# Optimization experiments

Measured on AMD Instinct MI355X. Metric: run time of the kernel, lower is better.

## Reference

```python
import jax, jax.numpy as jnp
import numpy as np

D_MODEL = 1024
NUM_HEADS = 16
D_K = D_MODEL // NUM_HEADS


def setup_inputs() -> dict:
    key = jax.random.key(0)
    ks = jax.random.split(key, 12)
    B, S = 2, 2048
    s = 1.0 / np.sqrt(D_MODEL)
    inp = {
        "query": jax.random.normal(ks[0], (B, S, D_MODEL), jnp.float32),
        "key": jax.random.normal(ks[1], (B, S, D_MODEL), jnp.float32),
        "value": jax.random.normal(ks[2], (B, S, D_MODEL), jnp.float32),
        "w_q": jax.random.normal(ks[3], (D_MODEL, D_MODEL), jnp.float32) * s,
        "b_q": jax.random.normal(ks[4], (D_MODEL,), jnp.float32) * 0.01,
        "w_k": jax.random.normal(ks[5], (D_MODEL, D_MODEL), jnp.float32) * s,
        "b_k": jax.random.normal(ks[6], (D_MODEL,), jnp.float32) * 0.01,
        "w_v": jax.random.normal(ks[7], (D_MODEL, D_MODEL), jnp.float32) * s,
        "b_v": jax.random.normal(ks[8], (D_MODEL,), jnp.float32) * 0.01,
        "w_o": jax.random.normal(ks[9], (D_MODEL, D_MODEL), jnp.float32) * s,
        "b_o": jax.random.normal(ks[10], (D_MODEL,), jnp.float32) * 0.01,
    }
    return inp


def _split_heads(x):
    # [B, S, d_model] -> [B, H, S, d_k]
    B, S, _ = x.shape
    return x.reshape(B, S, NUM_HEADS, D_K).transpose(0, 2, 1, 3)


def reference(query, key, value, w_q, b_q, w_k, b_k, w_v, b_v, w_o, b_o):
    B, S, _ = query.shape
    Q = _split_heads(query @ w_q.T + b_q)
    K = _split_heads(key @ w_k.T + b_k)
    V = _split_heads(value @ w_v.T + b_v)
    scale = 1.0 / jnp.sqrt(jnp.asarray(D_K, Q.dtype))
    scores = jnp.einsum("bhqd,bhkd->bhqk", Q, K) * scale  # [B,H,S,S]
    attn = jax.nn.softmax(scores, axis=-1)
    ctx = jnp.einsum("bhqk,bhkd->bhqd", attn, V)
    ctx = ctx.transpose(0, 2, 1, 3).reshape(B, S, D_MODEL)
    return ctx @ w_o.T + b_o
```

## Files before the change

### kernel.cpp

```cpp
#include <hip/hip_runtime.h>
#include <hip/hip_bf16.h>
#include <stdint.h>

#define D_MODEL 1024
#define NHEAD   16
#define DK      64
#define SEQ     2048
#define BATCH   2

using bf16 = __bf16;
typedef __bf16 bf16x8 __attribute__((ext_vector_type(8)));
typedef float  f32x4  __attribute__((ext_vector_type(4)));
typedef float  f32x16 __attribute__((ext_vector_type(16)));
typedef unsigned uintx2 __attribute__((ext_vector_type(2)));

__device__ __forceinline__ unsigned short f2bf(float x) {
  return __builtin_bit_cast(unsigned short, (__bf16)x);
}
__device__ __forceinline__ unsigned pk2bf(float a, float b) {
  return (unsigned)f2bf(a) | ((unsigned)f2bf(b) << 16);
}
__device__ __forceinline__ float uasf(unsigned x) {
  return __builtin_bit_cast(float, x);
}
__device__ __forceinline__ unsigned fasu(float x) {
  return __builtin_bit_cast(unsigned, x);
}

__device__ __forceinline__ void gld_lds16(const void* g, void* l) {
  __builtin_amdgcn_global_load_lds(
      (const __attribute__((address_space(1))) void*)g,
      (__attribute__((address_space(3))) void*)l, 16, 0, 0);
}

__device__ __forceinline__ float xhalf_sum(float x) {
  uintx2 r = __builtin_amdgcn_permlane32_swap(fasu(x), fasu(x), false, false);
  return uasf(r[0]) + uasf(r[1]);
}

#define MHA_PACK(sv, off, dst)                                           \
  {                                                                      \
    float e0 = __builtin_amdgcn_exp2f(sv[off + 0]);                      \
    float e1 = __builtin_amdgcn_exp2f(sv[off + 1]);                      \
    float e2 = __builtin_amdgcn_exp2f(sv[off + 2]);                      \
    float e3 = __builtin_amdgcn_exp2f(sv[off + 3]);                      \
    float e4 = __builtin_amdgcn_exp2f(sv[off + 4]);                      \
    float e5 = __builtin_amdgcn_exp2f(sv[off + 5]);                      \
    float e6 = __builtin_amdgcn_exp2f(sv[off + 6]);                      \
    float e7 = __builtin_amdgcn_exp2f(sv[off + 7]);                      \
    ps += ((e0 + e1) + (e2 + e3)) + ((e4 + e5) + (e6 + e7));             \
    unsigned c0 = pk2bf(e0, e1), c1 = pk2bf(e2, e3);                     \
    unsigned c2 = pk2bf(e4, e5), c3 = pk2bf(e6, e7);                     \
    uintx2 r02 = __builtin_amdgcn_permlane32_swap(c0, c2, false, false); \
    uintx2 r13 = __builtin_amdgcn_permlane32_swap(c1, c3, false, false); \
    uint4 w; w.x = r02[0]; w.y = r13[0]; w.z = r02[1]; w.w = r13[1];     \
    dst = __builtin_bit_cast(bf16x8, w);                                 \
  }

struct ConvArgs {
  const float* src[7];
  bf16* dst[7];
};

__global__ __launch_bounds__(256) void convert_f32_bf16(ConvArgs a) {
  int v = blockIdx.x * 256 + threadIdx.x;
  int seg, off;
  if (v < 3 * 1048576) { seg = v >> 20; off = v & (1048576 - 1); }
  else { int u = v - 3 * 1048576; seg = 3 + (u >> 18); off = u & (262144 - 1); }
  float4 f = ((const float4*)a.src[seg])[off];
  ushort4 o;
  o.x = f2bf(f.x); o.y = f2bf(f.y); o.z = f2bf(f.z); o.w = f2bf(f.w);
  ((ushort4*)a.dst[seg])[off] = o;
}

__device__ __forceinline__ void gemm_qkv_core(
    const bf16* __restrict__ A, const bf16* __restrict__ B,
    const float* __restrict__ bias, bf16* __restrict__ Cout,
    int mode, int bx, int by, float oscale, char* lds) {
  constexpr int BUF = 16384;
  constexpr int NKT = D_MODEL / 32;
  const int tid  = threadIdx.x;
  const int lane = tid & 63;
  const int wave = tid >> 6;
  const int wr = wave >> 1, wc = wave & 1;
  const int t = lane >> 4, q = lane & 15;

  f32x4 acc[4][4];
#pragma unroll
  for (int i = 0; i < 4; ++i)
#pragma unroll
    for (int j = 0; j < 4; ++j) acc[i][j] = (f32x4){0.f, 0.f, 0.f, 0.f};

  const char* Abase = (const char*)(A + (size_t)bx * 128 * D_MODEL);
  const char* Bbase = (const char*)(B + (size_t)by * 128 * D_MODEL);

  const char* gA[2]; char* sA[2]; const char* gB[2]; char* sB[2];
#pragma unroll
  for (int i = 0; i < 2; ++i) {
    int c = tid + i * 256, row = c >> 2;
    int src = ((c & 3) * 16) ^ ((row & 3) << 4);
    gA[i] = Abase + (size_t)row * (D_MODEL * 2) + src;
    sA[i] = lds + c * 16;
    gB[i] = Bbase + (size_t)row * (D_MODEL * 2) + src;
    sB[i] = lds + 8192 + c * 16;
  }

  const char* aA[4]; const char* aB[4];
#pragma unroll
  for (int f = 0; f < 4; ++f) {
    int ra = wr * 64 + f * 16 + q;
    aA[f] = lds + ra * 64 + ((t * 16) ^ ((q & 3) << 4));
    int rb = wc * 64 + f * 16 + q;
    aB[f] = lds + 8192 + rb * 64 + ((t * 16) ^ ((q & 3) << 4));
  }

#pragma unroll
  for (int i = 0; i < 2; ++i) { gld_lds16(gA[i], sA[i]); gld_lds16(gB[i], sB[i]); }
#pragma unroll
  for (int i = 0; i < 2; ++i) {
    gld_lds16(gA[i] + 64, sA[i] + BUF); gld_lds16(gB[i] + 64, sB[i] + BUF);
  }
  asm volatile("s_waitcnt vmcnt(4)" ::: "memory");
  __builtin_amdgcn_s_barrier();

#pragma unroll
  for (int kt = 0; kt < NKT; ++kt) {
    const int CUR = (kt % 3) * BUF;
    if (kt + 2 < NKT) {
      const int NB = ((kt + 2) % 3) * BUF;
#pragma unroll
      for (int i = 0; i < 2; ++i) {
        gld_lds16(gA[i] + (kt + 2) * 64, sA[i] + NB);
        gld_lds16(gB[i] + (kt + 2) * 64, sB[i] + NB);
      }
    }
    bf16x8 af[4], bfv[4];
#pragma unroll
    for (int f = 0; f < 4; ++f) af[f]  = *(const bf16x8*)(aA[f] + CUR);
#pragma unroll
    for (int f = 0; f < 4; ++f) bfv[f] = *(const bf16x8*)(aB[f] + CUR);
    __builtin_amdgcn_s_setprio(1);
#pragma unroll
    for (int fm = 0; fm < 4; ++fm)
#pragma unroll
      for (int fn = 0; fn < 4; ++fn)
        acc[fm][fn] = __builtin_amdgcn_mfma_f32_16x16x32_bf16(
            af[fm], bfv[fn], acc[fm][fn], 0, 0, 0);
    __builtin_amdgcn_s_setprio(0);
    if (kt + 2 < NKT)      asm volatile("s_waitcnt vmcnt(4)" ::: "memory");
    else if (kt + 1 < NKT) asm volatile("s_waitcnt vmcnt(0)" ::: "memory");
    __builtin_amdgcn_s_barrier();
  }

#pragma unroll
  for (int fm = 0; fm < 4; ++fm)
#pragma unroll
    for (int fn = 0; fn < 4; ++fn)
#pragma unroll
      for (int jj = 0; jj < 4; ++jj) {
        int m = bx * 128 + wr * 64 + fm * 16 + t * 4 + jj;
        int n = by * 128 + wc * 64 + fn * 16 + q;
        float v = acc[fm][fn][jj];
        if (mode == 0) {
          v = (v + bias[n]) * oscale;
          int b = m >> 11, s = m & (SEQ - 1), h = n >> 6, d = n & 63;
          Cout[(((size_t)(b * NHEAD + h)) * SEQ + s) * DK + d] = (bf16)v;
        } else {
          v += bias[m];
          int h = m >> 6, d = m & 63, b = n >> 11, s = n & (SEQ - 1);
          Cout[(((size_t)(b * NHEAD + h)) * DK + d) * SEQ + s] = (bf16)v;
        }
      }
}

struct QkvArgs {
  const bf16* A[3]; const bf16* B[3]; const float* bias[3]; bf16* out[3];
};

__global__ __launch_bounds__(256, 2) void gemm_qkv(QkvArgs a) {
  __shared__ char lds[3 * 16384];
  int z = blockIdx.z;
  int mode = (z == 2) ? 1 : 0;
  int bx = (z == 2) ? blockIdx.y : blockIdx.x;
  int by = (z == 2) ? blockIdx.x : blockIdx.y;
  float osc = (z == 0) ? 0.18033688011112042f : 1.0f;
  gemm_qkv_core(a.A[z], a.B[z], a.bias[z], a.out[z], mode, bx, by, osc, lds);
}

template <int BM>
__device__ __forceinline__ void gemm_core(
    const bf16* __restrict__ A, const bf16* __restrict__ B,
    const float* __restrict__ bias, float* __restrict__ Cout,
    int bx, int by, char* lds) {
  constexpr int FM   = BM / 32;
  constexpr int ACH  = BM / 32;
  constexpr int HALF = BM * 128 + 16384;
  const int tid  = threadIdx.x;
  const int lane = tid & 63;
  const int wave = tid >> 6;
  const int wr = wave >> 1, wc = wave & 1;
  const int t = lane >> 4, q = lane & 15;

  f32x4 acc[FM][4];
#pragma unroll
  for (int i = 0; i < FM; ++i)
#pragma unroll
    for (int j = 0; j < 4; ++j) acc[i][j] = (f32x4){0.f, 0.f, 0.f, 0.f};

  const char* Abase = (const char*)(A + (size_t)bx * BM * D_MODEL);
  const char* Bbase = (const char*)(B + (size_t)by * 128 * D_MODEL);

  const char* gA[ACH]; char* sA[ACH];
  const char* gB[4];   char* sB[4];
#pragma unroll
  for (int i = 0; i < ACH; ++i) {
    int c = tid + i * 256, row = c >> 3;
    int src = ((c & 7) * 16) ^ ((row & 7) << 4);
    gA[i] = Abase + (size_t)row * (D_MODEL * 2) + src;
    sA[i] = lds + c * 16;
  }
#pragma unroll
  for (int i = 0; i < 4; ++i) {
    int c = tid + i * 256, row = c >> 3;
    int src = ((c & 7) * 16) ^ ((row & 7) << 4);
    gB[i] = Bbase + (size_t)row * (D_MODEL * 2) + src;
    sB[i] = lds + BM * 128 + c * 16;
  }

  const char* aA[FM][2]; const char* aB[4][2];
#pragma unroll
  for (int f = 0; f < FM; ++f)
#pragma unroll
    for (int ks = 0; ks < 2; ++ks) {
      int ra = wr * (BM / 2) + f * 16 + q;
      aA[f][ks] = lds + ra * 128 + ((ks * 64 + t * 16) ^ ((q & 7) << 4));
    }
#pragma unroll
  for (int f = 0; f < 4; ++f)
#pragma unroll
    for (int ks = 0; ks < 2; ++ks) {
      int rb = wc * 64 + f * 16 + q;
      aB[f][ks] = lds + BM * 128 + rb * 128 + ((ks * 64 + t * 16) ^ ((q & 7) << 4));
    }

#pragma unroll
  for (int i = 0; i < ACH; ++i) gld_lds16(gA[i], sA[i]);
#pragma unroll
  for (int i = 0; i < 4; ++i)  gld_lds16(gB[i], sB[i]);
  __syncthreads();

  auto ktile = [&](int kt, int CUR) {
    if (kt + 1 < D_MODEL / 64) {
      int NXT = CUR ^ HALF;
#pragma unroll
      for (int i = 0; i < ACH; ++i) gld_lds16(gA[i] + (kt + 1) * 128, sA[i] + NXT);
#pragma unroll
      for (int i = 0; i < 4; ++i)  gld_lds16(gB[i] + (kt + 1) * 128, sB[i] + NXT);
    }
#pragma unroll
    for (int ks = 0; ks < 2; ++ks) {
      bf16x8 af[FM], bfv[4];
#pragma unroll
      for (int f = 0; f < FM; ++f) af[f] = *(const bf16x8*)(aA[f][ks] + CUR);
#pragma unroll
      for (int f = 0; f < 4; ++f)  bfv[f] = *(const bf16x8*)(aB[f][ks] + CUR);
      __builtin_amdgcn_s_setprio(1);
#pragma unroll
      for (int fm = 0; fm < FM; ++fm)
#pragma unroll
        for (int fn = 0; fn < 4; ++fn)
          acc[fm][fn] = __builtin_amdgcn_mfma_f32_16x16x32_bf16(
              af[fm], bfv[fn], acc[fm][fn], 0, 0, 0);
      __builtin_amdgcn_s_setprio(0);
    }
    __syncthreads();
  };
  for (int kt = 0; kt < D_MODEL / 64; kt += 2) {
    ktile(kt, 0);
    ktile(kt + 1, HALF);
  }

#pragma unroll
  for (int fm = 0; fm < FM; ++fm)
#pragma unroll
    for (int fn = 0; fn < 4; ++fn)
#pragma unroll
      for (int jj = 0; jj < 4; ++jj) {
        int m = bx * BM + wr * (BM / 2) + fm * 16 + t * 4 + jj;
        int n = by * 128 + wc * 64 + fn * 16 + q;
        Cout[(size_t)m * D_MODEL + n] = acc[fm][fn][jj] + bias[n];
      }
}

__global__ __launch_bounds__(256, 2) void gemm_o(
    const bf16* __restrict__ A, const bf16* __restrict__ B,
    const float* __restrict__ bias, float* __restrict__ Cout) {
  __shared__ char lds[2 * (64 * 128 + 16384)];
  gemm_core<64>(A, B, bias, Cout, blockIdx.x, blockIdx.y, lds);
}

__global__ __launch_bounds__(512, 2) void flash_attn(
    const bf16* __restrict__ Qh, const bf16* __restrict__ Kh,
    const bf16* __restrict__ Vt, bf16* __restrict__ ctx) {
  __shared__ char lds[65536];
  const int tid  = threadIdx.x;
  const int lane = tid & 63;
  const int wave = tid >> 6;
  const int lo = lane & 31;
  const int hi = lane >> 5;
  const int grp = wave >> 2;
  const int wq  = wave & 3;
  const int bh = blockIdx.x;
  const int q0 = blockIdx.y * 128 + wq * 32;

  const bf16* Qb = Qh + (size_t)bh * SEQ * DK;
  const char* Kb = (const char*)(Kh + (size_t)bh * SEQ * DK) + grp * 1024 * 128;
  const char* Vb = (const char*)(Vt + (size_t)bh * DK * SEQ) + grp * 1024 * 2;
  char* Kg = lds + grp * 16384;
  char* Vg = lds + 32768 + grp * 16384;

  bf16x8 qf[4];
#pragma unroll
  for (int c = 0; c < 4; ++c)
    qf[c] = *(const bf16x8*)(Qb + (size_t)(q0 + lo) * DK + c * 16 + hi * 8);

  const int tg = tid & 255;
  const int srow = tg >> 3;
  const int ssrc = ((tg & 7) * 16) ^ ((srow & 7) << 4);
  const char* gK0 = Kb + (size_t)srow * 128 + ssrc;
  const char* gK1 = Kb + (size_t)(srow + 32) * 128 + ssrc;
  const char* gV0 = Vb + (size_t)srow * 4096 + ssrc;
  const char* gV1 = Vb + (size_t)(srow + 32) * 4096 + ssrc;
  char* sK0 = Kg + tg * 16;
  char* sK1 = Kg + 4096 + tg * 16;
  char* sV0 = Vg + tg * 16;
  char* sV1 = Vg + 4096 + tg * 16;

  const int key = (lo & 7) << 4;
  const char* KA[4]; const char* VA[4];
#pragma unroll
  for (int c = 0; c < 4; ++c) {
    int o = (((2 * c + hi) * 16) ^ key) + lo * 128;
    KA[c] = Kg + o;
    VA[c] = Vg + o;
  }

  f32x16 acc0 = {}, acc1 = {};
  float lsum = 0.f;

  gld_lds16(gK0, sK0); gld_lds16(gK1, sK1);
  gld_lds16(gV0, sV0); gld_lds16(gV1, sV1);
  __syncthreads();

  auto tile = [&](int kt, int CUR) {
    if (kt + 1 < 16) {
      int nb = CUR ^ 8192;
      gld_lds16(gK0 + (kt + 1) * 8192, sK0 + nb);
      gld_lds16(gK1 + (kt + 1) * 8192, sK1 + nb);
      gld_lds16(gV0 + (kt + 1) * 128,  sV0 + nb);
      gld_lds16(gV1 + (kt + 1) * 128,  sV1 + nb);
    }

    float ps = 0.f;
    bf16x8 pa[4];

    {
      bf16x8 kf[4];
#pragma unroll
      for (int c = 0; c < 4; ++c) kf[c] = *(const bf16x8*)(KA[c] + CUR);
      f32x16 s0 = {};
      __builtin_amdgcn_s_setprio(1);
#pragma unroll
      for (int c = 0; c < 4; ++c)
        s0 = __builtin_amdgcn_mfma_f32_32x32x16_bf16(kf[c], qf[c], s0, 0, 0, 0);
      __builtin_amdgcn_s_setprio(0);
      MHA_PACK(s0, 0, pa[0]);
      MHA_PACK(s0, 8, pa[1]);
    }

    {
      bf16x8 kf[4];
#pragma unroll
      for (int c = 0; c < 4; ++c) kf[c] = *(const bf16x8*)(KA[c] + CUR + 4096);
      f32x16 s1 = {};
      __builtin_amdgcn_s_setprio(1);
#pragma unroll
      for (int c = 0; c < 4; ++c)
        s1 = __builtin_amdgcn_mfma_f32_32x32x16_bf16(kf[c], qf[c], s1, 0, 0, 0);
      __builtin_amdgcn_s_setprio(0);
      MHA_PACK(s1, 0, pa[2]);
      MHA_PACK(s1, 8, pa[3]);
    }
    lsum += ps;

    bf16x8 vf[2][4];
#pragma unroll
    for (int ks = 0; ks < 4; ++ks) {
      vf[0][ks] = *(const bf16x8*)(VA[ks] + CUR);
      vf[1][ks] = *(const bf16x8*)(VA[ks] + CUR + 4096);
    }
    __builtin_amdgcn_s_setprio(1);
#pragma unroll
    for (int ks = 0; ks < 4; ++ks) {
      acc0 = __builtin_amdgcn_mfma_f32_32x32x16_bf16(pa[ks], vf[0][ks], acc0, 0, 0, 0);
      acc1 = __builtin_amdgcn_mfma_f32_32x32x16_bf16(pa[ks], vf[1][ks], acc1, 0, 0, 0);
    }
    __builtin_amdgcn_s_setprio(0);

    __syncthreads();
  };

  for (int kt = 0; kt < 16; kt += 2) {
    tile(kt, 0);
    tile(kt + 1, 8192);
  }

  float lrun = xhalf_sum(lsum);

  float* lsh = (float*)lds;
  float* U1  = (float*)(lds + 4096);
  if (hi == 0) lsh[grp * 128 + wq * 32 + lo] = lrun;
  if (grp == 1) {
    float* dst = U1 + (size_t)(wq * 64 + lane) * 33;
#pragma unroll
    for (int r = 0; r < 16; ++r) { dst[r] = acc0[r]; dst[16 + r] = acc1[r]; }
  }
  __syncthreads();
  if (grp == 0) {
    const float* src = U1 + (size_t)(wq * 64 + lane) * 33;
    int b = bh >> 4, h = bh & 15;
#pragma unroll
    for (int r = 0; r < 16; ++r) {
      int row = (r & 3) + 8 * (r >> 2) + 4 * hi;
      int gr = wq * 32 + row;
      float linv = 1.f / (lsh[gr] + lsh[128 + gr]);
      float o0 = (acc0[r] + src[r]) * linv;
      float o1 = (acc1[r] + src[16 + r]) * linv;
      int srw = q0 + row;
      size_t base = ((size_t)(b * SEQ + srw)) * D_MODEL + h * 64 + lo;
      ctx[base]      = (bf16)o0;
      ctx[base + 32] = (bf16)o1;
    }
  }
}

extern "C" void kernel_launch(void* const* d_in, const int* in_sizes, int n_in,
                              void* d_out, int out_size, void* d_ws, size_t ws_size,
                              hipStream_t stream) {
  const float* query = (const float*)d_in[0];
  const float* key_  = (const float*)d_in[1];
  const float* value = (const float*)d_in[2];
  const float* w_q = (const float*)d_in[3];
  const float* b_q = (const float*)d_in[4];
  const float* w_k = (const float*)d_in[5];
  const float* b_k = (const float*)d_in[6];
  const float* w_v = (const float*)d_in[7];
  const float* b_v = (const float*)d_in[8];
  const float* w_o = (const float*)d_in[9];
  const float* b_o = (const float*)d_in[10];

  char* ws = (char*)d_ws;
  const size_t MB = 1024 * 1024;
  bf16* bQ  = (bf16*)(ws + 0 * MB);
  bf16* bK  = (bf16*)(ws + 8 * MB);
  bf16* bV  = (bf16*)(ws + 16 * MB);
  bf16* bWq = (bf16*)(ws + 24 * MB);
  bf16* bWk = (bf16*)(ws + 26 * MB);
  bf16* bWv = (bf16*)(ws + 28 * MB);
  bf16* bWo = (bf16*)(ws + 30 * MB);
  bf16* Qh  = (bf16*)(ws + 32 * MB);
  bf16* Kh  = (bf16*)(ws + 40 * MB);
  bf16* Vth = (bf16*)(ws + 48 * MB);
  bf16* ctx = (bf16*)(ws + 56 * MB);

  ConvArgs ca;
  ca.src[0] = query; ca.src[1] = key_; ca.src[2] = value;
  ca.src[3] = w_q;   ca.src[4] = w_k;  ca.src[5] = w_v; ca.src[6] = w_o;
  ca.dst[0] = bQ;  ca.dst[1] = bK;  ca.dst[2] = bV;
  ca.dst[3] = bWq; ca.dst[4] = bWk; ca.dst[5] = bWv; ca.dst[6] = bWo;
  convert_f32_bf16<<<16384, 256, 0, stream>>>(ca);

  QkvArgs qa;
  qa.A[0] = bQ;  qa.B[0] = bWq; qa.bias[0] = b_q; qa.out[0] = Qh;
  qa.A[1] = bK;  qa.B[1] = bWk; qa.bias[1] = b_k; qa.out[1] = Kh;
  qa.A[2] = bWv; qa.B[2] = bV;  qa.bias[2] = b_v; qa.out[2] = Vth;
  gemm_qkv<<<dim3(32, 8, 3), 256, 0, stream>>>(qa);

  flash_attn<<<dim3(32, 16), 512, 0, stream>>>(Qh, Kh, Vth, ctx);

  gemm_o<<<dim3(64, 8), 256, 0, stream>>>(ctx, bWo, b_o, (float*)d_out);
}
```

Measured before the change: 125.9 us.

## Triple-buffer output GEMM with BK=32 and split waitcnts in flash attention

The output projection GEMM now uses BK=32 tiles in a three-stage LDS ring, prefetching two tiles ahead, and waits with explicit vmcnt counts in place of full syncthreads drains. In flash attention, the K and V waits are split so the QK^T step only waits for K, and the V loads can still be in flight during the score MFMAs. This aims to hide global-to-LDS latency and remove the full memory drains at barriers. In exchange, the GEMM runs twice as many k-iterations with their barriers, and correctness now depends on exact counts of outstanding loads.

```diff
diff --git a/kernel.cpp b/kernel.cpp
--- a/kernel.cpp
+++ b/kernel.cpp
@@ -187,116 +187,98 @@
   gemm_qkv_core(a.A[z], a.B[z], a.bias[z], a.out[z], mode, bx, by, osc, lds);
 }
 
-template <int BM>
-__device__ __forceinline__ void gemm_core(
+__global__ __launch_bounds__(256, 2) void gemm_o(
     const bf16* __restrict__ A, const bf16* __restrict__ B,
-    const float* __restrict__ bias, float* __restrict__ Cout,
-    int bx, int by, char* lds) {
-  constexpr int FM   = BM / 32;
-  constexpr int ACH  = BM / 32;
-  constexpr int HALF = BM * 128 + 16384;
+    const float* __restrict__ bias, float* __restrict__ Cout) {
+  __shared__ char lds[3 * 12288];
+  constexpr int BUF = 12288;
+  constexpr int NKT = D_MODEL / 32;
   const int tid  = threadIdx.x;
   const int lane = tid & 63;
   const int wave = tid >> 6;
   const int wr = wave >> 1, wc = wave & 1;
   const int t = lane >> 4, q = lane & 15;
-
-  f32x4 acc[FM][4];
-#pragma unroll
-  for (int i = 0; i < FM; ++i)
+  const int bx = blockIdx.x, by = blockIdx.y;
+
+  f32x4 acc[2][4];
+#pragma unroll
+  for (int i = 0; i < 2; ++i)
 #pragma unroll
     for (int j = 0; j < 4; ++j) acc[i][j] = (f32x4){0.f, 0.f, 0.f, 0.f};
 
-  const char* Abase = (const char*)(A + (size_t)bx * BM * D_MODEL);
+  const char* Abase = (const char*)(A + (size_t)bx * 64 * D_MODEL);
   const char* Bbase = (const char*)(B + (size_t)by * 128 * D_MODEL);
 
-  const char* gA[ACH]; char* sA[ACH];
-  const char* gB[4];   char* sB[4];
-#pragma unroll
-  for (int i = 0; i < ACH; ++i) {
-    int c = tid + i * 256, row = c >> 3;
-    int src = ((c & 7) * 16) ^ ((row & 7) << 4);
-    gA[i] = Abase + (size_t)row * (D_MODEL * 2) + src;
-    sA[i] = lds + c * 16;
-  }
-#pragma unroll
-  for (int i = 0; i < 4; ++i) {
-    int c = tid + i * 256, row = c >> 3;
-    int src = ((c & 7) * 16) ^ ((row & 7) << 4);
+  const char* gA; char* sA; const char* gB[2]; char* sB[2];
+  {
+    int c = tid, row = c >> 2;
+    int src = ((c & 3) * 16) ^ ((row & 3) << 4);
+    gA = Abase + (size_t)row * (D_MODEL * 2) + src;
+    sA = lds + c * 16;
+  }
+#pragma unroll
+  for (int i = 0; i < 2; ++i) {
+    int c = tid + i * 256, row = c >> 2;
+    int src = ((c & 3) * 16) ^ ((row & 3) << 4);
     gB[i] = Bbase + (size_t)row * (D_MODEL * 2) + src;
-    sB[i] = lds + BM * 128 + c * 16;
-  }
-
-  const char* aA[FM][2]; const char* aB[4][2];
-#pragma unroll
-  for (int f = 0; f < FM; ++f)
-#pragma unroll
-    for (int ks = 0; ks < 2; ++ks) {
-      int ra = wr * (BM / 2) + f * 16 + q;
-      aA[f][ks] = lds + ra * 128 + ((ks * 64 + t * 16) ^ ((q & 7) << 4));
-    }
-#pragma unroll
-  for (int f = 0; f < 4; ++f)
-#pragma unroll
-    for (int ks = 0; ks < 2; ++ks) {
-      int rb = wc * 64 + f * 16 + q;
-      aB[f][ks] = lds + BM * 128 + rb * 128 + ((ks * 64 + t * 16) ^ ((q & 7) << 4));
-    }
-
-#pragma unroll
-  for (int i = 0; i < ACH; ++i) gld_lds16(gA[i], sA[i]);
-#pragma unroll
-  for (int i = 0; i < 4; ++i)  gld_lds16(gB[i], sB[i]);
-  __syncthreads();
-
-  auto ktile = [&](int kt, int CUR) {
-    if (kt + 1 < D_MODEL / 64) {
-      int NXT = CUR ^ HALF;
-#pragma unroll
-      for (int i = 0; i < ACH; ++i) gld_lds16(gA[i] + (kt + 1) * 128, sA[i] + NXT);
-#pragma unroll
-      for (int i = 0; i < 4; ++i)  gld_lds16(gB[i] + (kt + 1) * 128, sB[i] + NXT);
-    }
-#pragma unroll
-    for (int ks = 0; ks < 2; ++ks) {
-      bf16x8 af[FM], bfv[4];
-#pragma unroll
-      for (int f = 0; f < FM; ++f) af[f] = *(const bf16x8*)(aA[f][ks] + CUR);
-#pragma unroll
-      for (int f = 0; f < 4; ++f)  bfv[f] = *(const bf16x8*)(aB[f][ks] + CUR);
-      __builtin_amdgcn_s_setprio(1);
-#pragma unroll
-      for (int fm = 0; fm < FM; ++fm)
-#pragma unroll
-        for (int fn = 0; fn < 4; ++fn)
-          acc[fm][fn] = __builtin_amdgcn_mfma_f32_16x16x32_bf16(
-              af[fm], bfv[fn], acc[fm][fn], 0, 0, 0);
-      __builtin_amdgcn_s_setprio(0);
-    }
-    __syncthreads();
-  };
-  for (int kt = 0; kt < D_MODEL / 64; kt += 2) {
-    ktile(kt, 0);
-    ktile(kt + 1, HALF);
-  }
-
-#pragma unroll
-  for (int fm = 0; fm < FM; ++fm)
+    sB[i] = lds + 4096 + c * 16;
+  }
+
+  const char* aA[2]; const char* aB[4];
+#pragma unroll
+  for (int f = 0; f < 2; ++f) {
+    int ra = wr * 32 + f * 16 + q;
+    aA[f] = lds + ra * 64 + ((t * 16) ^ ((q & 3) << 4));
+  }
+#pragma unroll
+  for (int f = 0; f < 4; ++f) {
+    int rb = wc * 64 + f * 16 + q;
+    aB[f] = lds + 4096 + rb * 64 + ((t * 16) ^ ((q & 3) << 4));
+  }
+
+  gld_lds16(gA, sA); gld_lds16(gB[0], sB[0]); gld_lds16(gB[1], sB[1]);
+  gld_lds16(gA + 64, sA + BUF);
+  gld_lds16(gB[0] + 64, sB[0] + BUF); gld_lds16(gB[1] + 64, sB[1] + BUF);
+  asm volatile("s_waitcnt vmcnt(3)" ::: "memory");
+  __builtin_amdgcn_s_barrier();
+
+#pragma unroll
+  for (int kt = 0; kt < NKT; ++kt) {
+    const int CUR = (kt % 3) * BUF;
+    if (kt + 2 < NKT) {
+      const int NB = ((kt + 2) % 3) * BUF;
+      gld_lds16(gA + (kt + 2) * 64, sA + NB);
+      gld_lds16(gB[0] + (kt + 2) * 64, sB[0] + NB);
+      gld_lds16(gB[1] + (kt + 2) * 64, sB[1] + NB);
+    }
+    bf16x8 af[2], bfv[4];
+#pragma unroll
+    for (int f = 0; f < 2; ++f) af[f]  = *(const bf16x8*)(aA[f] + CUR);
+#pragma unroll
+    for (int f = 0; f < 4; ++f) bfv[f] = *(const bf16x8*)(aB[f] + CUR);
+    __builtin_amdgcn_s_setprio(1);
+#pragma unroll
+    for (int fm = 0; fm < 2; ++fm)
+#pragma unroll
+      for (int fn = 0; fn < 4; ++fn)
+        acc[fm][fn] = __builtin_amdgcn_mfma_f32_16x16x32_bf16(
+            af[fm], bfv[fn], acc[fm][fn], 0, 0, 0);
+    __builtin_amdgcn_s_setprio(0);
+    if (kt + 2 < NKT)      asm volatile("s_waitcnt vmcnt(3)" ::: "memory");
+    else if (kt + 1 < NKT) asm volatile("s_waitcnt vmcnt(0)" ::: "memory");
+    __builtin_amdgcn_s_barrier();
+  }
+
+#pragma unroll
+  for (int fm = 0; fm < 2; ++fm)
 #pragma unroll
     for (int fn = 0; fn < 4; ++fn)
 #pragma unroll
       for (int jj = 0; jj < 4; ++jj) {
-        int m = bx * BM + wr * (BM / 2) + fm * 16 + t * 4 + jj;
+        int m = bx * 64 + wr * 32 + fm * 16 + t * 4 + jj;
         int n = by * 128 + wc * 64 + fn * 16 + q;
         Cout[(size_t)m * D_MODEL + n] = acc[fm][fn][jj] + bias[n];
       }
-}
-
-__global__ __launch_bounds__(256, 2) void gemm_o(
-    const bf16* __restrict__ A, const bf16* __restrict__ B,
-    const float* __restrict__ bias, float* __restrict__ Cout) {
-  __shared__ char lds[2 * (64 * 128 + 16384)];
-  gemm_core<64>(A, B, bias, Cout, blockIdx.x, blockIdx.y, lds);
 }
 
 __global__ __launch_bounds__(512, 2) void flash_attn(
@@ -350,7 +332,8 @@
 
   gld_lds16(gK0, sK0); gld_lds16(gK1, sK1);
   gld_lds16(gV0, sV0); gld_lds16(gV1, sV1);
-  __syncthreads();
+  asm volatile("s_waitcnt vmcnt(2)" ::: "memory");
+  __builtin_amdgcn_s_barrier();
 
   auto tile = [&](int kt, int CUR) {
     if (kt + 1 < 16) {
@@ -393,6 +376,10 @@
     }
     lsum += ps;
 
+    if (kt + 1 < 16) asm volatile("s_waitcnt vmcnt(4)" ::: "memory");
+    else             asm volatile("s_waitcnt vmcnt(0)" ::: "memory");
+    __builtin_amdgcn_s_barrier();
+
     bf16x8 vf[2][4];
 #pragma unroll
     for (int ks = 0; ks < 4; ++ks) {
@@ -407,7 +394,8 @@
     }
     __builtin_amdgcn_s_setprio(0);
 
-    __syncthreads();
+    if (kt + 1 < 16) asm volatile("s_waitcnt vmcnt(2)" ::: "memory");
+    __builtin_amdgcn_s_barrier();
   };
 
   for (int kt = 0; kt < 16; kt += 2) {
```

Result: slower. 129.6 us (+3.0%).
